# Performance work log

Measured on AMD Instinct MI355X. Metric: run time of the kernel, lower is better.

Reference implementation:

```python
import jax, jax.numpy as jnp
import numpy as np

B = 1024       # batch_size b (features has 2*b rows)
DIM = 128      # feature dim
EPS = 1.0      # euclidean eps (module default)


def _make_neighbor_indices(b):
    # negative_samples (2048) >= 2*b - 1 -> deterministic full-batch branch
    idx = np.arange(b)
    not_self = ~np.eye(b, dtype=bool)
    neg1 = np.broadcast_to(idx[None, :], (b, b))[not_self].reshape(b, b - 1)
    neg2 = neg1 + b  # arange(b, 2b) excluding self position
    pos = (idx + b)[:, None]  # positive pair index, column 0
    return np.concatenate([pos, neg1, neg2], axis=1)  # [b, 2b-1]


def setup_inputs() -> dict:
    key = jax.random.key(0)
    features = jax.random.normal(key, (2 * B, DIM), dtype=jnp.float32)
    neigh_inds = jnp.asarray(_make_neighbor_indices(B), dtype=jnp.int64)
    return {"features": features, "neigh_inds": neigh_inds}


def reference(features, neigh_inds):
    b = features.shape[0] // 2
    neighbors = features[neigh_inds]            # [b, 2b-1, d] gather
    origs = features[:b]                        # [b, d]
    # squared euclidean distances anchor -> each neighbor
    dists = jnp.sum((origs[:, None, :] - neighbors) ** 2, axis=2)  # [b, 2b-1]
    probits = 1.0 / (EPS + dists)               # Cauchy kernel
    # infonce: positive is column 0 (clamp is (-inf, inf) -> identity)
    loss = -(jnp.log(probits[:, 0]) - jnp.log(jnp.sum(probits, axis=1)))
    return jnp.mean(loss)
```

## Files before the change

### kernel.cpp

```cpp
#include <hip/hip_runtime.h>
#include <hip/hip_bf16.h>

static constexpr int kB   = 1024;
static constexpr int kNF  = 2048;
static constexpr int kDIM = 128;

typedef __attribute__((ext_vector_type(8))) short  short8;
typedef __attribute__((ext_vector_type(4))) float  floatx4;

__global__ __launch_bounds__(256) void k_prep(const float* __restrict__ F,
                                              __hip_bfloat162* __restrict__ Fb2,
                                              float* __restrict__ norms,
                                              float* __restrict__ S,
                                              float* __restrict__ out) {
    const int t    = threadIdx.x;
    const int lane = t & 63;
    const int row  = blockIdx.x * 4 + (t >> 6);

    const float2 v = *(const float2*)(F + row * kDIM + lane * 2);

    __hip_bfloat162 bv;
    bv.x = __float2bfloat16(v.x);
    bv.y = __float2bfloat16(v.y);
    Fb2[row * (kDIM / 2) + lane] = bv;

    float n = v.x * v.x + v.y * v.y;
    #pragma unroll
    for (int off = 1; off < 64; off <<= 1) n += __shfl_xor(n, off, 64);
    if (lane == 0) norms[row] = n;

    if (blockIdx.x < 4) S[blockIdx.x * 256 + t] = 0.0f;
    if (blockIdx.x == 4 && t == 0) out[0] = 0.0f;
}

static constexpr int kLdsRow = kDIM + 8;

__global__ __launch_bounds__(256) void k_main(const unsigned short* __restrict__ Fb,
                                              const float* __restrict__ norms,
                                              float* __restrict__ S,
                                              float* __restrict__ P) {
    __shared__ unsigned short As[64 * kLdsRow];
    __shared__ unsigned short Bs[64 * kLdsRow];

    const int t  = threadIdx.x;
    const int i0 = blockIdx.x * 64;
    const int k0 = blockIdx.y * 64;

    #pragma unroll
    for (int e = 0; e < 4; ++e) {
        const int idx = e * 256 + t;
        const int row = idx >> 4;
        const int c   = idx & 15;
        const uint4 va = *(const uint4*)(Fb + (i0 + row) * kDIM + c * 8);
        const uint4 vb = *(const uint4*)(Fb + (k0 + row) * kDIM + c * 8);
        *(uint4*)(As + row * kLdsRow + c * 8) = va;
        *(uint4*)(Bs + row * kLdsRow + c * 8) = vb;
    }
    __syncthreads();

    const int lane = t & 63;
    const int w    = t >> 6;
    const int q    = lane >> 4;
    const int c    = lane & 15;

    floatx4 acc[4] = {{0.f,0.f,0.f,0.f},{0.f,0.f,0.f,0.f},
                      {0.f,0.f,0.f,0.f},{0.f,0.f,0.f,0.f}};

    const int arow = w * 16 + c;
    #pragma unroll
    for (int ks = 0; ks < 4; ++ks) {
        const short8 a = *(const short8*)(As + arow * kLdsRow + ks * 32 + q * 8);
        #pragma unroll
        for (int nt = 0; nt < 4; ++nt) {
            const short8 b = *(const short8*)(Bs + (nt * 16 + c) * kLdsRow + ks * 32 + q * 8);
            acc[nt] = __builtin_amdgcn_mfma_f32_16x16x32_bf16(a, b, acc[nt], 0, 0, 0);
        }
    }

    const int ibase = i0 + w * 16 + q * 4;
    float ni[4];
    #pragma unroll
    for (int r = 0; r < 4; ++r) ni[r] = norms[ibase + r];

    float psum[4] = {0.f, 0.f, 0.f, 0.f};
    #pragma unroll
    for (int nt = 0; nt < 4; ++nt) {
        const int   kg = k0 + nt * 16 + c;
        const float nk = norms[kg];
        #pragma unroll
        for (int r = 0; r < 4; ++r) {
            const int ig = ibase + r;
            float dist = ni[r] + nk - 2.0f * acc[nt][r];
            float p    = 1.0f / (1.0f + dist);
            if (kg == ig) p = 0.0f;
            psum[r] += p;
            if (kg == ig + kB) P[ig] = p;
        }
    }

    #pragma unroll
    for (int off = 1; off < 16; off <<= 1) {
        #pragma unroll
        for (int r = 0; r < 4; ++r) psum[r] += __shfl_xor(psum[r], off, 64);
    }
    if (c == 0) {
        #pragma unroll
        for (int r = 0; r < 4; ++r) atomicAdd(&S[ibase + r], psum[r]);
    }
}

__global__ __launch_bounds__(256) void k_final(const float* __restrict__ S,
                                               const float* __restrict__ P,
                                               float* __restrict__ out) {
    const int i = blockIdx.x * 256 + threadIdx.x;
    float l = __logf(S[i]) - __logf(P[i]);
    #pragma unroll
    for (int off = 1; off < 64; off <<= 1) l += __shfl_xor(l, off, 64);
    if ((threadIdx.x & 63) == 0) atomicAdd(out, l * (1.0f / (float)kB));
}

extern "C" void kernel_launch(void* const* d_in, const int* in_sizes, int n_in,
                              void* d_out, int out_size, void* d_ws, size_t ws_size,
                              hipStream_t stream) {
    const float* F = (const float*)d_in[0];
    float* out = (float*)d_out;

    char* ws = (char*)d_ws;
    unsigned short* Fb    = (unsigned short*)ws;
    float*          norms = (float*)(ws + 524288);
    float*          S     = (float*)(ws + 524288 + 8192);
    float*          P     = (float*)(ws + 524288 + 8192 + 4096);

    k_prep <<<dim3(512),    dim3(256), 0, stream>>>(F, (__hip_bfloat162*)Fb, norms, S, out);
    k_main <<<dim3(16, 32), dim3(256), 0, stream>>>(Fb, norms, S, P);
    k_final<<<dim3(4),      dim3(256), 0, stream>>>(S, P, out);
}
```

Measured before the change: 69.01 us.

## Fuse bf16 conversion and norms into main kernel, replace atomics with partial sums

Drops the separate prep kernel. The main kernel now loads fp32 features directly, converts them to bf16 into LDS and computes row norms in-block. The atomicAdd accumulation of row sums is replaced by per-column-block partial writes, which a single 1024-thread final block reduces deterministically without zero-initialisation. This removes one launch and the workspace round trip, at the cost of redundant fp32 loads and conversions across blocks.

```diff
diff --git a/kernel.cpp b/kernel.cpp
--- a/kernel.cpp
+++ b/kernel.cpp
@@ -2,59 +2,50 @@
 #include <hip/hip_bf16.h>
 
 static constexpr int kB   = 1024;
-static constexpr int kNF  = 2048;
 static constexpr int kDIM = 128;
+static constexpr int kLdsRow = kDIM + 8;
 
 typedef __attribute__((ext_vector_type(8))) short  short8;
 typedef __attribute__((ext_vector_type(4))) float  floatx4;
 
-__global__ __launch_bounds__(256) void k_prep(const float* __restrict__ F,
-                                              __hip_bfloat162* __restrict__ Fb2,
-                                              float* __restrict__ norms,
-                                              float* __restrict__ S,
-                                              float* __restrict__ out) {
-    const int t    = threadIdx.x;
-    const int lane = t & 63;
-    const int row  = blockIdx.x * 4 + (t >> 6);
-
-    const float2 v = *(const float2*)(F + row * kDIM + lane * 2);
-
-    __hip_bfloat162 bv;
-    bv.x = __float2bfloat16(v.x);
-    bv.y = __float2bfloat16(v.y);
-    Fb2[row * (kDIM / 2) + lane] = bv;
-
-    float n = v.x * v.x + v.y * v.y;
-    #pragma unroll
-    for (int off = 1; off < 64; off <<= 1) n += __shfl_xor(n, off, 64);
-    if (lane == 0) norms[row] = n;
-
-    if (blockIdx.x < 4) S[blockIdx.x * 256 + t] = 0.0f;
-    if (blockIdx.x == 4 && t == 0) out[0] = 0.0f;
+static __device__ inline unsigned short f2bf(float f) {
+    union { __hip_bfloat16 h; unsigned short u; } cv;
+    cv.h = __float2bfloat16(f);
+    return cv.u;
 }
 
-static constexpr int kLdsRow = kDIM + 8;
-
-__global__ __launch_bounds__(256) void k_main(const unsigned short* __restrict__ Fb,
-                                              const float* __restrict__ norms,
-                                              float* __restrict__ S,
+__global__ __launch_bounds__(256) void k_main(const float* __restrict__ F,
+                                              float* __restrict__ Spart,
                                               float* __restrict__ P) {
     __shared__ unsigned short As[64 * kLdsRow];
     __shared__ unsigned short Bs[64 * kLdsRow];
+    __shared__ float nI[64];
+    __shared__ float nK[64];
 
     const int t  = threadIdx.x;
     const int i0 = blockIdx.x * 64;
     const int k0 = blockIdx.y * 64;
 
-    #pragma unroll
-    for (int e = 0; e < 4; ++e) {
-        const int idx = e * 256 + t;
-        const int row = idx >> 4;
-        const int c   = idx & 15;
-        const uint4 va = *(const uint4*)(Fb + (i0 + row) * kDIM + c * 8);
-        const uint4 vb = *(const uint4*)(Fb + (k0 + row) * kDIM + c * 8);
-        *(uint4*)(As + row * kLdsRow + c * 8) = va;
-        *(uint4*)(Bs + row * kLdsRow + c * 8) = vb;
+    {
+        const int srow = t >> 2;
+        const int part = t & 3;
+        const float4* srcA = (const float4*)(F + (i0 + srow) * kDIM + part * 32);
+        const float4* srcB = (const float4*)(F + (k0 + srow) * kDIM + part * 32);
+        unsigned short* dA = As + srow * kLdsRow + part * 32;
+        unsigned short* dB = Bs + srow * kLdsRow + part * 32;
+        float na = 0.f, nb = 0.f;
+        #pragma unroll
+        for (int j = 0; j < 8; ++j) {
+            const float4 va = srcA[j];
+            const float4 vb = srcB[j];
+            na += va.x * va.x + va.y * va.y + va.z * va.z + va.w * va.w;
+            nb += vb.x * vb.x + vb.y * vb.y + vb.z * vb.z + vb.w * vb.w;
+            *(ushort4*)(dA + j * 4) = make_ushort4(f2bf(va.x), f2bf(va.y), f2bf(va.z), f2bf(va.w));
+            *(ushort4*)(dB + j * 4) = make_ushort4(f2bf(vb.x), f2bf(vb.y), f2bf(vb.z), f2bf(vb.w));
+        }
+        na += __shfl_xor(na, 1, 64); na += __shfl_xor(na, 2, 64);
+        nb += __shfl_xor(nb, 1, 64); nb += __shfl_xor(nb, 2, 64);
+        if (part == 0) { nI[srow] = na; nK[srow] = nb; }
     }
     __syncthreads();
 
@@ -80,18 +71,18 @@
     const int ibase = i0 + w * 16 + q * 4;
     float ni[4];
     #pragma unroll
-    for (int r = 0; r < 4; ++r) ni[r] = norms[ibase + r];
+    for (int r = 0; r < 4; ++r) ni[r] = nI[w * 16 + q * 4 + r];
 
     float psum[4] = {0.f, 0.f, 0.f, 0.f};
     #pragma unroll
     for (int nt = 0; nt < 4; ++nt) {
         const int   kg = k0 + nt * 16 + c;
-        const float nk = norms[kg];
+        const float nk = nK[nt * 16 + c];
         #pragma unroll
         for (int r = 0; r < 4; ++r) {
             const int ig = ibase + r;
-            float dist = ni[r] + nk - 2.0f * acc[nt][r];
-            float p    = 1.0f / (1.0f + dist);
+            const float dist = ni[r] + nk - 2.0f * acc[nt][r];
+            float p = 1.0f / (1.0f + dist);
             if (kg == ig) p = 0.0f;
             psum[r] += p;
             if (kg == ig + kB) P[ig] = p;
@@ -105,18 +96,33 @@
     }
     if (c == 0) {
         #pragma unroll
-        for (int r = 0; r < 4; ++r) atomicAdd(&S[ibase + r], psum[r]);
+        for (int r = 0; r < 4; ++r) Spart[(ibase + r) * 32 + blockIdx.y] = psum[r];
     }
 }
 
-__global__ __launch_bounds__(256) void k_final(const float* __restrict__ S,
-                                               const float* __restrict__ P,
-                                               float* __restrict__ out) {
-    const int i = blockIdx.x * 256 + threadIdx.x;
-    float l = __logf(S[i]) - __logf(P[i]);
+__global__ __launch_bounds__(1024) void k_final(const float* __restrict__ Spart,
+                                                const float* __restrict__ P,
+                                                float* __restrict__ out) {
+    __shared__ float red[16];
+    const int i = threadIdx.x;
+    const float4* sp = (const float4*)(Spart + i * 32);
+    float s = 0.f;
+    #pragma unroll
+    for (int j = 0; j < 8; ++j) {
+        const float4 v = sp[j];
+        s += v.x + v.y + v.z + v.w;
+    }
+    float l = __logf(s) - __logf(P[i]);
     #pragma unroll
     for (int off = 1; off < 64; off <<= 1) l += __shfl_xor(l, off, 64);
-    if ((threadIdx.x & 63) == 0) atomicAdd(out, l * (1.0f / (float)kB));
+    if ((i & 63) == 0) red[i >> 6] = l;
+    __syncthreads();
+    if (i < 16) {
+        float v = red[i];
+        #pragma unroll
+        for (int off = 1; off < 16; off <<= 1) v += __shfl_xor(v, off, 64);
+        if (i == 0) out[0] = v * (1.0f / (float)kB);
+    }
 }
 
 extern "C" void kernel_launch(void* const* d_in, const int* in_sizes, int n_in,
@@ -125,13 +131,10 @@
     const float* F = (const float*)d_in[0];
     float* out = (float*)d_out;
 
-    char* ws = (char*)d_ws;
-    unsigned short* Fb    = (unsigned short*)ws;
-    float*          norms = (float*)(ws + 524288);
-    float*          S     = (float*)(ws + 524288 + 8192);
-    float*          P     = (float*)(ws + 524288 + 8192 + 4096);
+    char*  ws    = (char*)d_ws;
+    float* Spart = (float*)ws;
+    float* P     = (float*)(ws + 131072);
 
-    k_prep <<<dim3(512),    dim3(256), 0, stream>>>(F, (__hip_bfloat162*)Fb, norms, S, out);
-    k_main <<<dim3(16, 32), dim3(256), 0, stream>>>(Fb, norms, S, P);
-    k_final<<<dim3(4),      dim3(256), 0, stream>>>(S, P, out);
+    k_main <<<dim3(16, 32), dim3(256), 0, stream>>>(F, Spart, P);
+    k_final<<<dim3(1),      dim3(1024), 0, stream>>>(Spart, P, out);
 }
```

Result: slower. 71.35 us (+3.4%).
